# Kernel optimization log

Measured on AMD Instinct MI355X. Metric: run time of the kernel, lower is better.

Reference implementation:

```python
import jax, jax.numpy as jnp
import numpy as np
from jax import lax

NUM_VARS = 16384
NUM_CHECKS = 8192
BATCH = 32
MAX_ITER = 15
H_DENSITY = 0.001  # ~8 ones per column, LDPC-like Tanner graph


def setup_inputs() -> dict:
    key = jax.random.key(0)
    k_h, k_s, k_l = jax.random.split(key, 3)
    # Sparse binary parity-check matrix represented densely (same math).
    parity_matrix = (jax.random.uniform(k_h, (NUM_CHECKS, NUM_VARS)) < H_DENSITY).astype(jnp.float32)
    syndrome = jax.random.randint(k_s, (BATCH, NUM_CHECKS), 0, 2).astype(jnp.float32)
    channel_llrs = jax.random.normal(k_l, (BATCH, NUM_VARS), dtype=jnp.float32)
    w_vc = jnp.ones((1,), dtype=jnp.float32)
    w_cv = jnp.ones((1,), dtype=jnp.float32)
    damping = jnp.float32(0.5)
    return {
        "syndrome": syndrome,
        "parity_matrix": parity_matrix,
        "channel_llrs": channel_llrs,
        "w_vc": w_vc,
        "w_cv": w_cv,
        "damping": damping,
    }


def reference(syndrome, parity_matrix, channel_llrs, w_vc, w_cv, damping):
    # syndrome: (B, C); parity_matrix H: (C, V); channel_llrs: (B, V)
    s_sign = 1.0 - 2.0 * syndrome  # (B, C)

    def body(v_beliefs, _):
        # v -> c: sparse.mm(H, v^T)^T == v @ H^T  -> (B, C)
        v_to_c = w_vc * (v_beliefs @ parity_matrix.T)
        c_msg = s_sign * jnp.tanh(v_to_c * 0.5)  # (B, C)
        # c -> v: sparse.mm(H^T, c^T)^T == c @ H  -> (B, V)
        c_to_v = w_cv * (c_msg @ parity_matrix)
        v_new = damping * v_beliefs + (1.0 - damping) * (channel_llrs + c_to_v)
        return v_new, None

    v_beliefs, _ = lax.scan(body, channel_llrs, None, length=MAX_ITER)
    return jax.nn.sigmoid(-v_beliefs)  # (B, V) bit-flip probabilities
```

## Files before the change

### kernel.cpp

```cpp
#include <hip/hip_runtime.h>


#define C_NUM 8192
#define V_NUM 16384
#define B_NUM 32
#define RW 64
#define CW 32

__global__ void build_csr(const float* __restrict__ H,
                          int* __restrict__ row_cnt, int* __restrict__ col_cnt,
                          int* __restrict__ row_idx, int* __restrict__ col_idx) {
    const long long total4 = (long long)C_NUM * V_NUM / 4;
    const long long stride = (long long)gridDim.x * blockDim.x;
    for (long long t = (long long)blockIdx.x * blockDim.x + threadIdx.x;
         t < total4; t += stride) {
        float4 hv = ((const float4*)H)[t];
        long long e = t * 4;
        float vals[4] = {hv.x, hv.y, hv.z, hv.w};
#pragma unroll
        for (int k = 0; k < 4; ++k) {
            if (vals[k] != 0.0f) {
                long long ee = e + k;
                int c = (int)(ee >> 14);
                int v = (int)(ee & (V_NUM - 1));
                int rs = atomicAdd(&row_cnt[c], 1);
                if (rs < RW) row_idx[c * RW + rs] = v;
                int cs = atomicAdd(&col_cnt[v], 1);
                if (cs < CW) col_idx[v * CW + cs] = c;
            }
        }
    }
}

__global__ void init_state(const float* __restrict__ llr,
                           const float* __restrict__ synd,
                           float* __restrict__ beliefs, float* __restrict__ llr_t,
                           float* __restrict__ ssign_t) {
    int t = blockIdx.x * blockDim.x + threadIdx.x;
    if (t < V_NUM * B_NUM) {
        int b = t & (B_NUM - 1);
        int v = t >> 5;
        float x = llr[b * V_NUM + v];
        beliefs[t] = x;
        llr_t[t] = x;
    }
    if (t < C_NUM * B_NUM) {
        int b = t & (B_NUM - 1);
        int c = t >> 5;
        ssign_t[t] = 1.0f - 2.0f * synd[b * C_NUM + c];
    }
}

__global__ void vc_kernel(const float* __restrict__ beliefs,
                          const int* __restrict__ row_cnt,
                          const int* __restrict__ row_idx,
                          const float* __restrict__ ssign_t,
                          const float* __restrict__ w_vc_p,
                          float* __restrict__ cmsg) {
    int t = blockIdx.x * blockDim.x + threadIdx.x;
    if (t >= C_NUM * B_NUM) return;
    int b = t & (B_NUM - 1);
    int c = t >> 5;
    float w = w_vc_p[0];
    int n = row_cnt[c];
    if (n > RW) n = RW;
    const int* __restrict__ idx = &row_idx[c * RW];
    float sum = 0.0f;
    for (int j = 0; j < n; ++j)
        sum += beliefs[idx[j] * B_NUM + b];
    cmsg[t] = ssign_t[t] * tanhf(0.5f * w * sum);
}

__global__ void cv_kernel(const float* __restrict__ cmsg,
                          const int* __restrict__ col_cnt,
                          const int* __restrict__ col_idx,
                          const float* __restrict__ llr_t,
                          const float* __restrict__ beliefs_in,
                          float* __restrict__ beliefs_out,
                          const float* __restrict__ w_cv_p,
                          const float* __restrict__ damping_p) {
    int t = blockIdx.x * blockDim.x + threadIdx.x;
    if (t >= V_NUM * B_NUM) return;
    int b = t & (B_NUM - 1);
    int v = t >> 5;
    float w = w_cv_p[0];
    float d = damping_p[0];
    int n = col_cnt[v];
    if (n > CW) n = CW;
    const int* __restrict__ idx = &col_idx[v * CW];
    float sum = 0.0f;
    for (int j = 0; j < n; ++j)
        sum += cmsg[idx[j] * B_NUM + b];
    beliefs_out[t] = d * beliefs_in[t] + (1.0f - d) * (llr_t[t] + w * sum);
}

__global__ void final_kernel(const float* __restrict__ beliefs,
                             float* __restrict__ out) {
    int t = blockIdx.x * blockDim.x + threadIdx.x;
    if (t >= V_NUM * B_NUM) return;
    int v = t & (V_NUM - 1);
    int b = t >> 14;
    float x = beliefs[v * B_NUM + b];
    out[t] = 1.0f / (1.0f + __expf(x));
}

extern "C" void kernel_launch(void* const* d_in, const int* in_sizes, int n_in,
                              void* d_out, int out_size, void* d_ws, size_t ws_size,
                              hipStream_t stream) {
    const float* synd = (const float*)d_in[0];
    const float* H    = (const float*)d_in[1];
    const float* llr  = (const float*)d_in[2];
    const float* w_vc = (const float*)d_in[3];
    const float* w_cv = (const float*)d_in[4];
    const float* damp = (const float*)d_in[5];
    float* out = (float*)d_out;

    char* ws = (char*)d_ws;
    size_t off = 0;
    int* row_cnt = (int*)(ws + off); off += (size_t)C_NUM * 4;
    int* col_cnt = (int*)(ws + off); off += (size_t)V_NUM * 4;
    int* row_idx = (int*)(ws + off); off += (size_t)C_NUM * RW * 4;
    int* col_idx = (int*)(ws + off); off += (size_t)V_NUM * CW * 4;
    float* beliefs_a = (float*)(ws + off); off += (size_t)V_NUM * B_NUM * 4;
    float* beliefs_b = (float*)(ws + off); off += (size_t)V_NUM * B_NUM * 4;
    float* cmsg      = (float*)(ws + off); off += (size_t)C_NUM * B_NUM * 4;
    float* ssign_t   = (float*)(ws + off); off += (size_t)C_NUM * B_NUM * 4;
    float* llr_t     = (float*)(ws + off); off += (size_t)V_NUM * B_NUM * 4;

    hipMemsetAsync(row_cnt, 0, (size_t)(C_NUM + V_NUM) * 4, stream);

    build_csr<<<8192, 256, 0, stream>>>(H, row_cnt, col_cnt, row_idx, col_idx);
    init_state<<<(V_NUM * B_NUM + 255) / 256, 256, 0, stream>>>(
        llr, synd, beliefs_a, llr_t, ssign_t);

    float* cur = beliefs_a;
    float* nxt = beliefs_b;
    for (int it = 0; it < 15; ++it) {
        vc_kernel<<<(C_NUM * B_NUM + 255) / 256, 256, 0, stream>>>(
            cur, row_cnt, row_idx, ssign_t, w_vc, cmsg);
        cv_kernel<<<(V_NUM * B_NUM + 255) / 256, 256, 0, stream>>>(
            cmsg, col_cnt, col_idx, llr_t, cur, nxt, w_cv, damp);
        float* tmp = cur; cur = nxt; nxt = tmp;
    }
    final_kernel<<<(V_NUM * B_NUM + 255) / 256, 256, 0, stream>>>(cur, out);
}
```

Measured before the change: 1.094 ms.

## Fuse CSR build with state init, vectorize index loads, use fast tanh

Merges the CSR construction and state initialisation kernels into one grid-stride launch, saving one kernel launch. The gather loops in the check and variable updates now load neighbour indices as int4 and do four gathers per step, giving more memory-level parallelism. tanhf is replaced by an exp-based formula, bounds checks are dropped, and 64-bit index math becomes 32-bit. The dominant cost is still streaming the 512MB dense H matrix, so the overall effect is probably small, and the fast tanh slightly changes numerics.

```diff
diff --git a/kernel.cpp b/kernel.cpp
--- a/kernel.cpp
+++ b/kernel.cpp
@@ -7,22 +7,40 @@
 #define RW 64
 #define CW 32
 
-__global__ void build_csr(const float* __restrict__ H,
-                          int* __restrict__ row_cnt, int* __restrict__ col_cnt,
-                          int* __restrict__ row_idx, int* __restrict__ col_idx) {
-    const long long total4 = (long long)C_NUM * V_NUM / 4;
-    const long long stride = (long long)gridDim.x * blockDim.x;
-    for (long long t = (long long)blockIdx.x * blockDim.x + threadIdx.x;
-         t < total4; t += stride) {
+__global__ void build_and_init(const float* __restrict__ H,
+                               const float* __restrict__ llr,
+                               const float* __restrict__ synd,
+                               int* __restrict__ row_cnt, int* __restrict__ col_cnt,
+                               int* __restrict__ row_idx, int* __restrict__ col_idx,
+                               float* __restrict__ beliefs, float* __restrict__ llr_t,
+                               float* __restrict__ ssign_t) {
+    const int tid = blockIdx.x * blockDim.x + threadIdx.x;
+    const int nth = gridDim.x * blockDim.x;
+
+    for (int t = tid; t < V_NUM * B_NUM; t += nth) {
+        int b = t & (B_NUM - 1);
+        int v = t >> 5;
+        float x = llr[b * V_NUM + v];
+        beliefs[t] = x;
+        llr_t[t] = x;
+    }
+    for (int t = tid; t < C_NUM * B_NUM; t += nth) {
+        int b = t & (B_NUM - 1);
+        int c = t >> 5;
+        ssign_t[t] = 1.0f - 2.0f * synd[b * C_NUM + c];
+    }
+
+    const int total4 = C_NUM * V_NUM / 4;
+    for (int t = tid; t < total4; t += nth) {
         float4 hv = ((const float4*)H)[t];
-        long long e = t * 4;
+        int e = t * 4;
         float vals[4] = {hv.x, hv.y, hv.z, hv.w};
 #pragma unroll
         for (int k = 0; k < 4; ++k) {
             if (vals[k] != 0.0f) {
-                long long ee = e + k;
-                int c = (int)(ee >> 14);
-                int v = (int)(ee & (V_NUM - 1));
+                int ee = e + k;
+                int c = ee >> 14;
+                int v = ee & (V_NUM - 1);
                 int rs = atomicAdd(&row_cnt[c], 1);
                 if (rs < RW) row_idx[c * RW + rs] = v;
                 int cs = atomicAdd(&col_cnt[v], 1);
@@ -32,72 +50,71 @@
     }
 }
 
-__global__ void init_state(const float* __restrict__ llr,
-                           const float* __restrict__ synd,
-                           float* __restrict__ beliefs, float* __restrict__ llr_t,
-                           float* __restrict__ ssign_t) {
-    int t = blockIdx.x * blockDim.x + threadIdx.x;
-    if (t < V_NUM * B_NUM) {
-        int b = t & (B_NUM - 1);
-        int v = t >> 5;
-        float x = llr[b * V_NUM + v];
-        beliefs[t] = x;
-        llr_t[t] = x;
-    }
-    if (t < C_NUM * B_NUM) {
-        int b = t & (B_NUM - 1);
-        int c = t >> 5;
-        ssign_t[t] = 1.0f - 2.0f * synd[b * C_NUM + c];
-    }
+__device__ __forceinline__ float fast_tanh_half(float x) {
+    float ax = fabsf(x);
+    float e = __expf(-ax);
+    float th = (1.0f - e) / (1.0f + e);
+    return copysignf(th, x);
 }
 
-__global__ void vc_kernel(const float* __restrict__ beliefs,
+__global__ void vc_kernel(const float* __restrict__ cur,
                           const int* __restrict__ row_cnt,
                           const int* __restrict__ row_idx,
                           const float* __restrict__ ssign_t,
                           const float* __restrict__ w_vc_p,
                           float* __restrict__ cmsg) {
     int t = blockIdx.x * blockDim.x + threadIdx.x;
-    if (t >= C_NUM * B_NUM) return;
     int b = t & (B_NUM - 1);
     int c = t >> 5;
-    float w = w_vc_p[0];
     int n = row_cnt[c];
     if (n > RW) n = RW;
-    const int* __restrict__ idx = &row_idx[c * RW];
+    const int4* __restrict__ idx4 = (const int4*)&row_idx[c * RW];
     float sum = 0.0f;
-    for (int j = 0; j < n; ++j)
-        sum += beliefs[idx[j] * B_NUM + b];
-    cmsg[t] = ssign_t[t] * tanhf(0.5f * w * sum);
+    int k4 = (n + 3) >> 2;
+    for (int k = 0; k < k4; ++k) {
+        int4 q = idx4[k];
+        int j = 4 * k;
+        float s0 = (j     < n) ? cur[q.x * B_NUM + b] : 0.0f;
+        float s1 = (j + 1 < n) ? cur[q.y * B_NUM + b] : 0.0f;
+        float s2 = (j + 2 < n) ? cur[q.z * B_NUM + b] : 0.0f;
+        float s3 = (j + 3 < n) ? cur[q.w * B_NUM + b] : 0.0f;
+        sum += (s0 + s1) + (s2 + s3);
+    }
+    cmsg[t] = ssign_t[t] * fast_tanh_half(w_vc_p[0] * sum);
 }
 
 __global__ void cv_kernel(const float* __restrict__ cmsg,
                           const int* __restrict__ col_cnt,
                           const int* __restrict__ col_idx,
                           const float* __restrict__ llr_t,
-                          const float* __restrict__ beliefs_in,
-                          float* __restrict__ beliefs_out,
+                          const float* __restrict__ cur,
+                          float* __restrict__ nxt,
                           const float* __restrict__ w_cv_p,
-                          const float* __restrict__ damping_p) {
+                          const float* __restrict__ damp_p) {
     int t = blockIdx.x * blockDim.x + threadIdx.x;
-    if (t >= V_NUM * B_NUM) return;
     int b = t & (B_NUM - 1);
     int v = t >> 5;
-    float w = w_cv_p[0];
-    float d = damping_p[0];
     int n = col_cnt[v];
     if (n > CW) n = CW;
-    const int* __restrict__ idx = &col_idx[v * CW];
+    const int4* __restrict__ idx4 = (const int4*)&col_idx[v * CW];
     float sum = 0.0f;
-    for (int j = 0; j < n; ++j)
-        sum += cmsg[idx[j] * B_NUM + b];
-    beliefs_out[t] = d * beliefs_in[t] + (1.0f - d) * (llr_t[t] + w * sum);
+    int k4 = (n + 3) >> 2;
+    for (int k = 0; k < k4; ++k) {
+        int4 q = idx4[k];
+        int j = 4 * k;
+        float s0 = (j     < n) ? cmsg[q.x * B_NUM + b] : 0.0f;
+        float s1 = (j + 1 < n) ? cmsg[q.y * B_NUM + b] : 0.0f;
+        float s2 = (j + 2 < n) ? cmsg[q.z * B_NUM + b] : 0.0f;
+        float s3 = (j + 3 < n) ? cmsg[q.w * B_NUM + b] : 0.0f;
+        sum += (s0 + s1) + (s2 + s3);
+    }
+    float d = damp_p[0];
+    nxt[t] = d * cur[t] + (1.0f - d) * (llr_t[t] + w_cv_p[0] * sum);
 }
 
 __global__ void final_kernel(const float* __restrict__ beliefs,
                              float* __restrict__ out) {
     int t = blockIdx.x * blockDim.x + threadIdx.x;
-    if (t >= V_NUM * B_NUM) return;
     int v = t & (V_NUM - 1);
     int b = t >> 14;
     float x = beliefs[v * B_NUM + b];
@@ -129,18 +146,18 @@
 
     hipMemsetAsync(row_cnt, 0, (size_t)(C_NUM + V_NUM) * 4, stream);
 
-    build_csr<<<8192, 256, 0, stream>>>(H, row_cnt, col_cnt, row_idx, col_idx);
-    init_state<<<(V_NUM * B_NUM + 255) / 256, 256, 0, stream>>>(
-        llr, synd, beliefs_a, llr_t, ssign_t);
+    build_and_init<<<8192, 256, 0, stream>>>(H, llr, synd,
+                                             row_cnt, col_cnt, row_idx, col_idx,
+                                             beliefs_a, llr_t, ssign_t);
 
     float* cur = beliefs_a;
     float* nxt = beliefs_b;
     for (int it = 0; it < 15; ++it) {
-        vc_kernel<<<(C_NUM * B_NUM + 255) / 256, 256, 0, stream>>>(
+        vc_kernel<<<(C_NUM * B_NUM) / 256, 256, 0, stream>>>(
             cur, row_cnt, row_idx, ssign_t, w_vc, cmsg);
-        cv_kernel<<<(V_NUM * B_NUM + 255) / 256, 256, 0, stream>>>(
+        cv_kernel<<<(V_NUM * B_NUM) / 256, 256, 0, stream>>>(
             cmsg, col_cnt, col_idx, llr_t, cur, nxt, w_cv, damp);
         float* tmp = cur; cur = nxt; nxt = tmp;
     }
-    final_kernel<<<(V_NUM * B_NUM + 255) / 256, 256, 0, stream>>>(cur, out);
+    final_kernel<<<(V_NUM * B_NUM) / 256, 256, 0, stream>>>(cur, out);
 }
```

After: 1.012 ms. 1.08x faster.
